# Kernel tuning notes

Measured on AMD Instinct MI355X. Metric: run time of the kernel, lower is better.

The kernel has to match this reference:

```python
import jax, jax.numpy as jnp
import numpy as np

B, LI, LT, D, H, DH, E, I, IS, TOPK = 2, 1024, 256, 768, 12, 64, 8, 3072, 1536, 2


def _rms(x, s):
    # RMSNorm over last dim, eps=1e-6, learned scale s [DH]
    r = jax.lax.rsqrt(jnp.mean(x * x, axis=-1, keepdims=True) + 1e-6)
    return x * r * s


def _ln(x):
    # LayerNorm without affine (elementwise_affine=False), eps=1e-6
    m = jnp.mean(x, axis=-1, keepdims=True)
    v = jnp.mean((x - m) ** 2, axis=-1, keepdims=True)
    return (x - m) * jax.lax.rsqrt(v + 1e-6)


def _mlp(x, wg, wu, wd):
    # SwiGLU MoeMLP: down(silu(gate(x)) * up(x))
    return (jax.nn.silu(x @ wg.T) * (x @ wu.T)) @ wd.T


def _moe(x, gw, eg, eu, ed, sg, su, sd):
    # x: [T, D]. Softmax gate -> top-k (norm_topk_prob=False -> raw weights),
    # combine expert outputs weighted by routing probs, plus shared experts.
    scores = jax.nn.softmax(x @ gw.T, axis=-1)            # [T, E]
    tw, ti = jax.lax.top_k(scores, TOPK)                  # [T, K]
    T = x.shape[0]
    w = jnp.zeros((T, E), x.dtype).at[jnp.arange(T)[:, None], ti].add(tw)
    y = jnp.zeros_like(x)
    for e in range(E):  # fixed small expert count
        y = y + w[:, e:e + 1] * _mlp(x, eg[e], eu[e], ed[e])
    return y + _mlp(x, sg, su, sd)


def _mod(vec, w, b):
    # Modulation(double=True): Linear(silu(vec)) -> 6 chunks, broadcast over seq
    return jnp.split((jax.nn.silu(vec) @ w.T + b)[:, None, :], 6, axis=-1)


def _qkv(x, w, b, qs, ks):
    Bb, L, _ = x.shape
    qkv = (x @ w.T + b).reshape(Bb, L, 3, H, DH).transpose(2, 0, 3, 1, 4)  # [3,B,H,L,DH]
    q, k, v = qkv[0], qkv[1], qkv[2]
    return _rms(q, qs), _rms(k, ks), v


def _forward(img, txt, vec, imw, imb, tmw, tmb, iqkvw, iqkvb, ipw, ipb, tqkvw, tqkvb, tpw, tpb, iqs, iks, tqs, tks, igw, ieg, ieu, ied, isg, isu, isd, tgw, teg, teu, ted, tsg, tsu, tsd):
    is1, ic1, ig1, is2, ic2, ig2 = _mod(vec, imw, imb)
    ts1, tc1, tg1, ts2, tc2, tg2 = _mod(vec, tmw, tmb)
    iq, ik, iv = _qkv((1 + ic1) * _ln(img) + is1, iqkvw, iqkvb, iqs, iks)
    tq, tk, tv = _qkv((1 + tc1) * _ln(txt) + ts1, tqkvw, tqkvb, tqs, tks)
    # joint attention over concat(txt, img)
    q = jnp.concatenate([tq, iq], axis=2)
    k = jnp.concatenate([tk, ik], axis=2)
    v = jnp.concatenate([tv, iv], axis=2)
    a = jax.nn.softmax(jnp.einsum('bhqd,bhkd->bhqk', q, k) / np.float32(np.sqrt(DH)), axis=-1)
    o = jnp.einsum('bhqk,bhkd->bhqd', a, v).transpose(0, 2, 1, 3).reshape(B, LT + LI, D)
    txt_a, img_a = o[:, :LT], o[:, LT:]
    img = img + ig1 * (img_a @ ipw.T + ipb)
    txt = txt + tg1 * (txt_a @ tpw.T + tpb)
    img = img + ig2 * _moe(((1 + ic2) * _ln(img) + is2).reshape(-1, D), igw, ieg, ieu, ied, isg, isu, isd).reshape(B, LI, D)
    txt = txt + tg2 * _moe(((1 + tc2) * _ln(txt) + ts2).reshape(-1, D), tgw, teg, teu, ted, tsg, tsu, tsd).reshape(B, LT, D)
    return img, txt


def setup_inputs() -> dict:
    key = jax.random.key(0)
    ks = jax.random.split(key, 32)
    n = lambda i, sh, s=1.0: jax.random.normal(ks[i], sh, jnp.float32) * s
    W = 0.02
    return {
        'img': n(0, (B, LI, D)), 'txt': n(1, (B, LT, D)), 'vec': n(2, (B, D)),
        'imw': n(3, (6 * D, D), W), 'imb': n(4, (6 * D,), W),
        'tmw': n(5, (6 * D, D), W), 'tmb': n(6, (6 * D,), W),
        'iqkvw': n(7, (3 * D, D), W), 'iqkvb': n(8, (3 * D,), W),
        'ipw': n(9, (D, D), W), 'ipb': n(10, (D,), W),
        'tqkvw': n(11, (3 * D, D), W), 'tqkvb': n(12, (3 * D,), W),
        'tpw': n(13, (D, D), W), 'tpb': n(14, (D,), W),
        'iqs': jnp.ones((DH,), jnp.float32), 'iks': jnp.ones((DH,), jnp.float32),
        'tqs': jnp.ones((DH,), jnp.float32), 'tks': jnp.ones((DH,), jnp.float32),
        'igw': n(15, (E, D), W), 'ieg': n(16, (E, I, D), W), 'ieu': n(17, (E, I, D), W), 'ied': n(18, (E, D, I), W),
        'isg': n(19, (IS, D), W), 'isu': n(20, (IS, D), W), 'isd': n(21, (D, IS), W),
        'tgw': n(22, (E, D), W), 'teg': n(23, (E, I, D), W), 'teu': n(24, (E, I, D), W), 'ted': n(25, (E, D, I), W),
        'tsg': n(26, (IS, D), W), 'tsu': n(27, (IS, D), W), 'tsd': n(28, (D, IS), W),
    }


def reference(img, txt, vec, imw, imb, tmw, tmb, iqkvw, iqkvb, ipw, ipb, tqkvw, tqkvb, tpw, tpb, iqs, iks, tqs, tks, igw, ieg, ieu, ied, isg, isu, isd, tgw, teg, teu, ted, tsg, tsu, tsd):
    return _forward(img, txt, vec, imw, imb, tmw, tmb, iqkvw, iqkvb, ipw, ipb, tqkvw, tqkvb, tpw, tpb, iqs, iks, tqs, tks, igw, ieg, ieu, ied, isg, isu, isd, tgw, teg, teu, ted, tsg, tsu, tsd)
```

## Files before the change

### kernel.cpp

```cpp
#include <hip/hip_runtime.h>
#include <hip/hip_bf16.h>

using bf16 = __hip_bfloat16;
typedef __attribute__((ext_vector_type(4))) float f32x4;
typedef __attribute__((ext_vector_type(8))) short s16x8;

#define DEV static __device__ __forceinline__
DEV float bf2f(bf16 x){ return __bfloat162float(x); }
DEV bf16  f2bf(float x){ return __float2bfloat16(x); }
DEV float silu_(float x){ return x / (1.f + expf(-x)); }

template<bool B_F32, bool EXPERT, bool GATHER, int OUT, bool BIAS, bool GU>
DEV void gemm_core(
    const bf16* __restrict__ A, const void* __restrict__ Bv,
    const void* __restrict__ B2v,
    const float* __restrict__ bias, void* __restrict__ C,
    int M, int N, int K, long a_zoff, long b_zoff, int bshift, int biasz,
    int zdiv, long c_so, long c_si, int ldc,
    float alpha, int ksplit, long c_spo,
    const int* __restrict__ rowlist, const int* __restrict__ offsets,
    const int* __restrict__ counts)
{
  __shared__ __align__(16) char smem_[36864];
  bf16 (*As)[72] = (bf16(*)[72])smem_;
  bf16 (*Bs)[72] = (bf16(*)[72])(smem_ + 18432);
  float (*st)[132] = (float(*)[132])smem_;

  const int zz = blockIdx.z;
  const int z = zz / ksplit, split = zz % ksplit;
  const int m0 = blockIdx.y * 128, n0 = blockIdx.x * 128;
  int Meff = M; long rowbase = 0;
  if (EXPERT){ Meff = counts[z]; rowbase = offsets[z]; }
  if (m0 >= Meff) return;
  const bf16* Ab = A + (EXPERT ? 0 : z * a_zoff);
  const int bidx = z >> bshift;
  long coff;
  if (EXPERT) coff = rowbase * (long)ldc;
  else        coff = (long)(z / zdiv) * c_so + (long)(z % zdiv) * c_si;
  coff += (long)split * c_spo;
  const float* bias_eff = BIAS ? bias + (long)bidx * biasz : nullptr;

  const int klen = K / ksplit;
  const int kbeg = split * klen;
  const int NT = klen >> 6;

  const int tid = threadIdx.x;
  const int lane = tid & 63, wid = tid >> 6;
  const int wm = wid >> 1, wn = wid & 1;

  const int rbase = tid >> 3;
  const int kc = (tid & 7) << 3;
  const bf16* ap[4];
  const bf16* bp[4];  const float* bpf[4];
  const bf16* bp2[4]; const float* bpf2[4];
  bool avalid[4], bvalid[4];
  #pragma unroll
  for (int it = 0; it < 4; it++){
    int row = rbase + 32 * it;
    long ar = 0;
    if (EXPERT){
      int i = m0 + row;
      avalid[it] = i < Meff;
      if (avalid[it]) ar = GATHER ? (long)rowlist[rowbase + i] : (rowbase + i);
    } else {
      avalid[it] = (m0 + row) < Meff;
      ar = m0 + row;
    }
    ap[it] = Ab + ar * (long)K + kbeg + kc;
    bvalid[it] = (n0 + row) < N;
    long br = bvalid[it] ? (long)(n0 + row) : 0;
    if (B_F32){
      bpf[it] = (const float*)Bv + bidx * b_zoff + br * K + kbeg + kc;
      if (GU) bpf2[it] = (const float*)B2v + bidx * b_zoff + br * K + kbeg + kc;
    } else {
      bp[it]  = (const bf16*)Bv + bidx * b_zoff + br * K + kbeg + kc;
      if (GU) bp2[it] = (const bf16*)B2v + bidx * b_zoff + br * K + kbeg + kc;
    }
  }

  uint4 ra[4], rb[4], rb2[4];
  float4 fb0[4], fb1[4], f20[4], f21[4];
  const uint4 zero4 = make_uint4(0u,0u,0u,0u);

  auto LOADA = [&](int koff){
    #pragma unroll
    for (int it = 0; it < 4; it++)
      ra[it] = avalid[it] ? *(const uint4*)(ap[it] + koff) : zero4;
  };
  auto LOADB = [&](int koff){
    #pragma unroll
    for (int it = 0; it < 4; it++){
      if (B_F32){
        if (bvalid[it]){ fb0[it] = *(const float4*)(bpf[it] + koff);
                         fb1[it] = *(const float4*)(bpf[it] + koff + 4); }
        else { fb0[it] = make_float4(0,0,0,0); fb1[it] = make_float4(0,0,0,0); }
      } else rb[it] = bvalid[it] ? *(const uint4*)(bp[it] + koff) : zero4;
    }
  };
  auto LOADB2 = [&](int koff){
    #pragma unroll
    for (int it = 0; it < 4; it++){
      if (B_F32){
        if (bvalid[it]){ f20[it] = *(const float4*)(bpf2[it] + koff);
                         f21[it] = *(const float4*)(bpf2[it] + koff + 4); }
        else { f20[it] = make_float4(0,0,0,0); f21[it] = make_float4(0,0,0,0); }
      } else rb2[it] = bvalid[it] ? *(const uint4*)(bp2[it] + koff) : zero4;
    }
  };
  auto cvt = [&](float4 a, float4 b)->uint4{
    union { bf16 h[8]; uint4 v; } u;
    u.h[0]=f2bf(a.x); u.h[1]=f2bf(a.y); u.h[2]=f2bf(a.z); u.h[3]=f2bf(a.w);
    u.h[4]=f2bf(b.x); u.h[5]=f2bf(b.y); u.h[6]=f2bf(b.z); u.h[7]=f2bf(b.w);
    return u.v;
  };
  auto STOREA = [&](){
    #pragma unroll
    for (int it = 0; it < 4; it++) *(uint4*)(&As[rbase + 32*it][kc]) = ra[it];
  };
  auto STOREB = [&](){
    #pragma unroll
    for (int it = 0; it < 4; it++)
      *(uint4*)(&Bs[rbase + 32*it][kc]) = B_F32 ? cvt(fb0[it], fb1[it]) : rb[it];
  };
  auto STOREB2 = [&](){
    #pragma unroll
    for (int it = 0; it < 4; it++)
      *(uint4*)(&Bs[rbase + 32*it][kc]) = B_F32 ? cvt(f20[it], f21[it]) : rb2[it];
  };

  f32x4 acc[4][4] = {};
  f32x4 acc2[4][4] = {};
  auto MFMA = [&](f32x4 (&ac)[4][4]){
    #pragma unroll
    for (int ks2 = 0; ks2 < 2; ks2++){
      const int r16 = lane & 15;
      const int kk = ks2 * 32 + ((lane >> 4) << 3);
      s16x8 af[4], bfr[4];
      #pragma unroll
      for (int mi = 0; mi < 4; mi++) af[mi]  = *(const s16x8*)(&As[wm*64 + mi*16 + r16][kk]);
      #pragma unroll
      for (int ni = 0; ni < 4; ni++) bfr[ni] = *(const s16x8*)(&Bs[wn*64 + ni*16 + r16][kk]);
      #pragma unroll
      for (int mi = 0; mi < 4; mi++)
        #pragma unroll
        for (int ni = 0; ni < 4; ni++)
          ac[mi][ni] = __builtin_amdgcn_mfma_f32_16x16x32_bf16(af[mi], bfr[ni], ac[mi][ni], 0, 0, 0);
    }
  };

  LOADA(0); LOADB(0);
  for (int t = 0; t < NT; t++){
    STOREA(); STOREB();
    __syncthreads();
    if (GU){
      LOADB2(t << 6);
      MFMA(acc);
      __syncthreads();
      STOREB2();
      __syncthreads();
      if (t + 1 < NT){ LOADA((t+1) << 6); LOADB((t+1) << 6); }
      MFMA(acc2);
      __syncthreads();
    } else {
      if (t + 1 < NT){ LOADA((t+1) << 6); LOADB((t+1) << 6); }
      MFMA(acc);
      __syncthreads();
    }
  }

  const int er = tid >> 3;
  const int ec = (tid & 7) << 4;
  const int erg = m0 + (er & 15) + ((er & 16) ? 64 : 0);
  #pragma unroll
  for (int mi = 0; mi < 4; mi++){
    #pragma unroll
    for (int ni = 0; ni < 4; ni++){
      int lc = wn*64 + ni*16 + (lane & 15);
      float bv = 0.f;
      if (BIAS){ if (split == 0) bv = bias_eff[n0 + lc]; }
      #pragma unroll
      for (int i = 0; i < 4; i++){
        int lr = wm*16 + ((lane >> 4) << 2) + i;
        float v;
        if (GU) v = silu_(acc[mi][ni][i]) * acc2[mi][ni][i];
        else    v = acc[mi][ni][i] * alpha + bv;
        st[lr][lc] = v;
      }
    }
    __syncthreads();
    int rg = erg + mi*16;
    int cg = n0 + ec;
    if (rg < Meff && cg < N){
      long base = coff + (long)rg * ldc + cg;
      if (OUT == 0){
        float* dst = (float*)C + base;
        #pragma unroll
        for (int q = 0; q < 4; q++)
          *(float4*)(dst + 4*q) = make_float4(st[er][ec+4*q], st[er][ec+4*q+1],
                                              st[er][ec+4*q+2], st[er][ec+4*q+3]);
      } else {
        union { bf16 h[8]; uint4 v; } o0, o1;
        #pragma unroll
        for (int j = 0; j < 8; j++){
          o0.h[j] = f2bf(st[er][ec+j]);
          o1.h[j] = f2bf(st[er][ec+8+j]);
        }
        *(uint4*)((bf16*)C + base)     = o0.v;
        *(uint4*)((bf16*)C + base + 8) = o1.v;
      }
    }
    __syncthreads();
  }
}

#define GEMM_K(NAME, BF32, EXPERT, GATHER, OUT, BIAS, GU)                          \
__global__ __launch_bounds__(256) void NAME(                                       \
    const bf16* A, const void* Bv, const void* B2v, const float* bias, void* C,    \
    int M, int N, int K, long az, long bz, int bshift, int biasz,                  \
    int zdiv, long cso, long csi, int ldc, float alpha, int ks, long cspo,         \
    const int* rl, const int* ofs, const int* cnt){                                \
  gemm_core<BF32,EXPERT,GATHER,OUT,BIAS,GU>(A,Bv,B2v,bias,C,M,N,K,az,bz,bshift,    \
      biasz,zdiv,cso,csi,ldc,alpha,ks,cspo,rl,ofs,cnt); }

GEMM_K(k_qkv_b,  false,true ,false,1,true ,false)
GEMM_K(k_qkt,    false,false,false,1,false,false)
GEMM_K(k_pv,     false,false,false,0,false,false)
GEMM_K(k_proj_b, false,true ,false,0,true ,false)
GEMM_K(k_gu_b,   false,true ,true ,1,false,true )
GEMM_K(k_down_b, false,true ,false,0,false,false)
GEMM_K(k_sgu_b,  false,true ,false,1,false,true )
GEMM_K(k_sdown_b,false,true ,false,0,false,false)
GEMM_K(k_qkv_f,  true ,true ,false,1,true ,false)
GEMM_K(k_proj_f, true ,true ,false,0,true ,false)
GEMM_K(k_gu_f,   true ,true ,true ,1,false,true )
GEMM_K(k_down_f, true ,true ,false,0,false,false)
GEMM_K(k_sgu_f,  true ,true ,false,1,false,true )
GEMM_K(k_sdown_f,true ,true ,false,0,false,false)

__global__ void init_kernel(int* cnt16, int* tabs){
  int i = threadIdx.x;
  if (i < 16) cnt16[i] = 0;
  if (i == 0){
    tabs[0]=2048; tabs[1]=512; tabs[2]=0; tabs[3]=2048;
    tabs[4]=256; tabs[5]=256; tabs[6]=1024; tabs[7]=1024;
    tabs[8]=0; tabs[9]=1280; tabs[10]=256; tabs[11]=1536;
    tabs[12]=2048; tabs[13]=512; tabs[14]=0; tabs[15]=2048;
  }
}
__global__ void tables_kernel(const int* cnt16, int* ofs16, int* cur16){
  if (threadIdx.x == 0){
    int o = 0;
    for (int e = 0; e < 8; e++){ ofs16[e] = o; o += cnt16[e]; cur16[e] = 0; }
    o = 4096;
    for (int e = 8; e < 16; e++){ ofs16[e] = o; o += cnt16[e]; cur16[e] = 0; }
  }
}

__global__ __launch_bounds__(256) void f2b_kernel(const float* __restrict__ in,
    bf16* __restrict__ out, long n){
  long i = ((long)blockIdx.x * 256 + threadIdx.x) * 8;
  if (i >= n) return;
  float4 a = *(const float4*)(in + i);
  float4 b = *(const float4*)(in + i + 4);
  union { bf16 h[8]; uint4 v; } u;
  u.h[0]=f2bf(a.x); u.h[1]=f2bf(a.y); u.h[2]=f2bf(a.z); u.h[3]=f2bf(a.w);
  u.h[4]=f2bf(b.x); u.h[5]=f2bf(b.y); u.h[6]=f2bf(b.z); u.h[7]=f2bf(b.w);
  *(uint4*)(out + i) = u.v;
}

__global__ __launch_bounds__(256) void reduce_o_kernel(const float* __restrict__ Op,
    bf16* __restrict__ O, int chunk){
  int z = blockIdx.y;
  int bh = chunk*6 + z;
  int b = bh / 12, hh = bh % 12;
  int d = threadIdx.x & 63, rr = threadIdx.x >> 6;
  const float* base = Op + (long)z * 1280 * 64;
  #pragma unroll
  for (int j = 0; j < 4; j++){
    int row = blockIdx.x * 16 + rr * 4 + j;
    float s = 0.f;
    #pragma unroll
    for (int sp = 0; sp < 10; sp++) s += base[(long)sp*6*1280*64 + (long)row*64 + d];
    O[((long)b*1280 + row)*768 + hh*64 + d] = f2bf(s);
  }
}

__global__ __launch_bounds__(256) void mod_kernel(const float* __restrict__ vec,
    const float* __restrict__ w, const float* __restrict__ b, float* __restrict__ out){
  int bb = blockIdx.y;
  __shared__ float sv[768];
  int tid = threadIdx.x;
  for (int i = tid; i < 768; i += 256){ float v = vec[bb*768 + i]; sv[i] = v/(1.f+expf(-v)); }
  __syncthreads();
  int w4 = tid >> 6, lane = tid & 63;
  int j0 = blockIdx.x * 8 + w4 * 2;
  for (int jj = 0; jj < 2; jj++){
    int j = j0 + jj;
    const float* wr = w + (long)j * 768;
    float p = 0.f;
    #pragma unroll
    for (int i = 0; i < 12; i++) p += sv[lane + 64*i] * wr[lane + 64*i];
    for (int o = 32; o; o >>= 1) p += __shfl_xor(p, o);
    if (lane == 0) out[bb*4608 + j] = p + b[j];
  }
}
// ... 156 lines not shown

__global__ __launch_bounds__(256) void scatter_kernel(const int* __restrict__ tki,
    const int* __restrict__ ofs16, int* __restrict__ cur16,
    int* __restrict__ rows16, int* __restrict__ tpos, int T, int tabofs, int rowadd){
  int idx = blockIdx.x * 256 + threadIdx.x;
  if (idx >= T * 2) return;
  int t = idx >> 1;
  int e = tki[idx];
  int pos = atomicAdd(&cur16[tabofs + e], 1);
  int g = ofs16[tabofs + e] + pos;
  rows16[g] = rowadd + t;
  tpos[idx] = g;
}

__global__ __launch_bounds__(256) void combine_kernel(const float* __restrict__ h,
    const float* __restrict__ mod, const float* __restrict__ tkw, const int* __restrict__ tpos,
    const float* __restrict__ ye, long espo, const float* __restrict__ ys, long sspo,
    float* __restrict__ out, int L){
  int t = blockIdx.x; int b = t / L;
  const float* g2 = mod + (long)b * 4608 + 5*768;
  float w0 = tkw[t*2], w1 = tkw[t*2+1];
  long p0 = (long)tpos[t*2] * 768, p1 = (long)tpos[t*2+1] * 768;
  for (int d = threadIdx.x; d < 768; d += 256){
    float e0 = ye[p0+d] + ye[espo+p0+d];
    float e1 = ye[p1+d] + ye[espo+p1+d];
    float sv = ys[(long)t*768+d] + ys[sspo+(long)t*768+d];
    out[(long)t*768 + d] = h[(long)t*768 + d] + g2[d] * (w0*e0 + w1*e1 + sv);
  }
}

extern "C" void kernel_launch(void* const* d_in, const int* in_sizes, int n_in,
                              void* d_out, int out_size, void* d_ws, size_t ws_size,
                              hipStream_t stream){
  (void)in_sizes; (void)n_in; (void)out_size;
  const float* fin[33];
  for (int i = 0; i < 33; i++) fin[i] = (const float*)d_in[i];
  float* out_img = (float*)d_out;
  float* out_txt = (float*)d_out + (long)2*1024*768;

  char* ws = (char*)d_ws;
  size_t off = 0, peak = 0;
  auto alloc = [&](size_t n)->char*{
    off = (off + 255) & ~(size_t)255;
    char* p = ws + off; off += n;
    if (off > peak) peak = off;
    return p;
  };

  float *mod_i, *mod_t, *h_i, *h_t, *x2fc, *tkw_i, *tkw_t;
  bf16 *x2c;
  int *tki_i, *tki_t, *cnt16, *ofs16, *cur16, *rows16, *tpos_i, *tpos_t, *tabs;
  float *qb_ws, *pb_ws;
  bf16 *wq=nullptr,*wp=nullptr,*wg16=nullptr,*wu16=nullptr,*wd16=nullptr,
       *wsg2=nullptr,*wsu2=nullptr,*wsd2=nullptr;
  bf16 *Qb,*Kb,*Vt,*O,*xmc,*qrc,*S,*P;
  float *pjc,*Opart;
  bf16 *h1,*h1s;
  float *ye,*ys;

  auto build = [&](bool W){
    off = 0; peak = 0;
    mod_i=(float*)alloc(2*4608*4);  mod_t=(float*)alloc(2*4608*4);
    h_i  =(float*)alloc((size_t)2048*768*4); h_t=(float*)alloc((size_t)512*768*4);
    x2c  =(bf16*) alloc((size_t)2560*768*2);
    x2fc =(float*)alloc((size_t)2560*768*4);
    tkw_i=(float*)alloc(2048*2*4); tki_i=(int*)alloc(2048*2*4);
    tkw_t=(float*)alloc(512*2*4);  tki_t=(int*)alloc(512*2*4);
    cnt16=(int*)alloc(16*4); ofs16=(int*)alloc(16*4); cur16=(int*)alloc(16*4);
    rows16=(int*)alloc(5120*4);
    tpos_i=(int*)alloc(4096*4); tpos_t=(int*)alloc(1024*4);
    tabs=(int*)alloc(64*4);
    qb_ws=(float*)alloc(2*2304*4); pb_ws=(float*)alloc(2*768*4);
    if (W){
      const size_t EB = (size_t)8*3072*768*2;
      wg16=(bf16*)alloc(2*EB); wu16=(bf16*)alloc(2*EB); wd16=(bf16*)alloc(2*EB);
      wq  =(bf16*)alloc(2*(size_t)2304*768*2);
      wp  =(bf16*)alloc(2*(size_t)768*768*2);
      wsg2=(bf16*)alloc(2*(size_t)1536*768*2);
      wsu2=(bf16*)alloc(2*(size_t)1536*768*2);
      wsd2=(bf16*)alloc(2*(size_t)768*1536*2);
    }
    size_t arena = (off + 255) & ~(size_t)255;
    off = arena;
    Qb=(bf16*)alloc((size_t)24*1280*64*2);
    Kb=(bf16*)alloc((size_t)24*1280*64*2);
    Vt=(bf16*)alloc((size_t)24*1280*64*2);
    O =(bf16*)alloc((size_t)2*1280*768*2);
    pjc=(float*)alloc((size_t)2*2560*768*4);
    size_t sub = (off + 255) & ~(size_t)255;
    xmc=(bf16*)alloc((size_t)2560*768*2);
    qrc=(bf16*)alloc((size_t)2560*2304*2);
    off = sub;
    S=(bf16*)alloc((size_t)6*1280*1280*2);
    P=(bf16*)alloc((size_t)6*1280*1280*2);
    Opart=(float*)alloc((size_t)10*6*1280*64*4);
    off = arena;
    h1 =(bf16*) alloc((size_t)5120*3072*2);
    ye =(float*)alloc((size_t)2*5120*768*4);
    h1s=(bf16*) alloc((size_t)2560*1536*2);
    ys =(float*)alloc((size_t)2*2560*768*4);
  };

  build(true);
  bool W = (peak <= ws_size);
  if (!W) build(false);

  hipMemcpyAsync(qb_ws,        fin[8],  2304*4, hipMemcpyDeviceToDevice, stream);
  hipMemcpyAsync(qb_ws+2304,   fin[12], 2304*4, hipMemcpyDeviceToDevice, stream);
  hipMemcpyAsync(pb_ws,        fin[14], 768*4,  hipMemcpyDeviceToDevice, stream);
  hipMemcpyAsync(pb_ws+768,    fin[10], 768*4,  hipMemcpyDeviceToDevice, stream);

  if (W){
    auto cv = [&](const float* src, bf16* dst, long n){
      f2b_kernel<<<(unsigned)((n/8 + 255)/256), 256, 0, stream>>>(src, dst, n);
    };
    const long EN = (long)8*3072*768;
    cv(fin[20], wg16, EN);      cv(fin[27], wg16+EN, EN);
    cv(fin[21], wu16, EN);      cv(fin[28], wu16+EN, EN);
    cv(fin[22], wd16, EN);      cv(fin[29], wd16+EN, EN);
    cv(fin[7],  wq, (long)2304*768);   cv(fin[11], wq+(long)2304*768, (long)2304*768);
    cv(fin[13], wp, (long)768*768);    cv(fin[9],  wp+(long)768*768,  (long)768*768);
    cv(fin[23], wsg2, (long)1536*768); cv(fin[30], wsg2+(long)1536*768, (long)1536*768);
    cv(fin[24], wsu2, (long)1536*768); cv(fin[31], wsu2+(long)1536*768, (long)1536*768);
    cv(fin[25], wsd2, (long)768*1536); cv(fin[32], wsd2+(long)768*1536, (long)768*1536);
  }

  init_kernel<<<1, 64, 0, stream>>>(cnt16, tabs);
  mod_kernel<<<dim3(576,2), 256, 0, stream>>>(fin[2], fin[3], fin[4], mod_i);
  mod_kernel<<<dim3(576,2), 256, 0, stream>>>(fin[2], fin[5], fin[6], mod_t);
  ln_mod_kernel<<<2048, 256, 0, stream>>>(fin[0], mod_i, xmc, 1024);
  ln_mod_kernel<<<512,  256, 0, stream>>>(fin[1], mod_t, xmc + (long)2048*768, 256);

  if (W)
    k_qkv_b<<<dim3(18,16,2), 256, 0, stream>>>(xmc, wq, nullptr, qb_ws, qrc,
        0, 2304, 768, 0, (long)2304*768, 0, 2304, 1, 0, 0, 2304, 1.f, 1, 0,
        nullptr, tabs+2, tabs+0);
  else {
    k_qkv_f<<<dim3(18,16,1), 256, 0, stream>>>(xmc, fin[7], nullptr, qb_ws, qrc,
        0, 2304, 768, 0, 0, 0, 0, 1, 0, 0, 2304, 1.f, 1, 0, nullptr, tabs+2, tabs+0);
    k_qkv_f<<<dim3(18,4,1), 256, 0, stream>>>(xmc, fin[11], nullptr, qb_ws+2304, qrc,
        0, 2304, 768, 0, 0, 0, 0, 1, 0, 0, 2304, 1.f, 1, 0, nullptr, tabs+3, tabs+1);
  }
  qkv_scatter_kernel<<<dim3(16,24), 256, 0, stream>>>(qrc, fin[15], fin[16], Qb, Kb, Vt, 1024, 256);
  qkv_scatter_kernel<<<dim3(4,24),  256, 0, stream>>>(qrc + (long)2048*2304, fin[17], fin[18], Qb, Kb, Vt, 256, 0);

  for (int ch = 0; ch < 4; ch++){
    const bf16* Qc = Qb + (size_t)ch * 6 * 1280 * 64;
    const bf16* Kc = Kb + (size_t)ch * 6 * 1280 * 64;
    const bf16* Vc = Vt + (size_t)ch * 6 * 1280 * 64;
    k_qkt<<<dim3(10,10,6), 256, 0, stream>>>(Qc, Kc, nullptr, nullptr, S,
        1280, 1280, 64, (long)1280*64, (long)1280*64, 0, 0,
        1, (long)1280*1280, 0, 1280, 0.125f, 1, 0, nullptr, nullptr, nullptr);
    softmax_kernel<<<6*1280, 256, 0, stream>>>(S, P);
    k_pv<<<dim3(1,10,60), 256, 0, stream>>>(P, Vc, nullptr, nullptr, Opart,
        1280, 64, 1280, (long)1280*1280, (long)64*1280, 0, 0,
        1, (long)1280*64, 0, 64, 1.f, 10, (long)6*1280*64, nullptr, nullptr, nullptr);
    reduce_o_kernel<<<dim3(80,6), 256, 0, stream>>>(Opart, O, ch);
  }

  if (W)
    k_proj_b<<<dim3(6,8,8), 256, 0, stream>>>(O, wp, nullptr, pb_ws, pjc,
        0, 768, 768, 0, (long)768*768, 1, 768, 1, 0, 0, 768, 1.f, 2, (long)2560*768,
        nullptr, tabs+8, tabs+4);
  else {
    k_proj_f<<<dim3(6,2,4), 256, 0, stream>>>(O, fin[13], nullptr, pb_ws, pjc,
        0, 768, 768, 0, 0, 1, 0, 1, 0, 0, 768, 1.f, 2, (long)2560*768,
        nullptr, tabs+8, tabs+4);
    k_proj_f<<<dim3(6,8,4), 256, 0, stream>>>(O, fin[9], nullptr, pb_ws+768, pjc,
        0, 768, 768, 0, 0, 1, 0, 1, 0, 0, 768, 1.f, 2, (long)2560*768,
        nullptr, tabs+10, tabs+6);
  }
  resid_ln_mod_kernel<<<2048, 256, 0, stream>>>(fin[0], pjc, 256, (long)2560*768,
      mod_i, h_i, x2c, x2fc, 1024);
  resid_ln_mod_kernel<<<512, 256, 0, stream>>>(fin[1], pjc, 0, (long)2560*768,
      mod_t, h_t, x2c + (long)2048*768, x2fc + (long)2048*768, 256);

  router_kernel<<<512, 256, 0, stream>>>(x2fc, fin[19], tkw_i, tki_i, cnt16, 2048);
  router_kernel<<<128, 256, 0, stream>>>(x2fc + (long)2048*768, fin[26], tkw_t, tki_t, cnt16+8, 512);
  tables_kernel<<<1, 1, 0, stream>>>(cnt16, ofs16, cur16);
  scatter_kernel<<<16, 256, 0, stream>>>(tki_i, ofs16, cur16, rows16, tpos_i, 2048, 0, 0);
  scatter_kernel<<<4,  256, 0, stream>>>(tki_t, ofs16, cur16, rows16, tpos_t, 512, 8, 2048);

  if (W){
    k_gu_b<<<dim3(24,16,16), 256, 0, stream>>>(x2c, wg16, wu16, nullptr, h1,
        0, 3072, 768, 0, (long)3072*768, 0, 0, 1, 0, 0, 3072, 1.f, 1, 0,
        rows16, ofs16, cnt16);
    k_down_b<<<dim3(6,16,32), 256, 0, stream>>>(h1, wd16, nullptr, nullptr, ye,
        0, 768, 3072, 0, (long)768*3072, 0, 0, 1, 0, 0, 768, 1.f, 2, (long)5120*768,
        nullptr, ofs16, cnt16);
    k_sgu_b<<<dim3(12,16,2), 256, 0, stream>>>(x2c, wsg2, wsu2, nullptr, h1s,
        0, 1536, 768, 0, (long)1536*768, 0, 0, 1, 0, 0, 1536, 1.f, 1, 0,
        nullptr, tabs+14, tabs+12);
    k_sdown_b<<<dim3(6,16,4), 256, 0, stream>>>(h1s, wsd2, nullptr, nullptr, ys,
        0, 768, 1536, 0, (long)768*1536, 0, 0, 1, 0, 0, 768, 1.f, 2, (long)2560*768,
        nullptr, tabs+14, tabs+12);
  } else {
    k_gu_f<<<dim3(24,16,8), 256, 0, stream>>>(x2c, fin[20], fin[21], nullptr, h1,
        0, 3072, 768, 0, (long)3072*768, 0, 0, 1, 0, 0, 3072, 1.f, 1, 0,
        rows16, ofs16, cnt16);
    k_gu_f<<<dim3(24,16,8), 256, 0, stream>>>(x2c, fin[27], fin[28], nullptr, h1,
        0, 3072, 768, 0, (long)3072*768, 0, 0, 1, 0, 0, 3072, 1.f, 1, 0,
        rows16, ofs16+8, cnt16+8);
    k_down_f<<<dim3(6,16,16), 256, 0, stream>>>(h1, fin[22], nullptr, nullptr, ye,
        0, 768, 3072, 0, (long)768*3072, 0, 0, 1, 0, 0, 768, 1.f, 2, (long)5120*768,
        nullptr, ofs16, cnt16);
    k_down_f<<<dim3(6,16,16), 256, 0, stream>>>(h1, fin[29], nullptr, nullptr, ye,
        0, 768, 3072, 0, (long)768*3072, 0, 0, 1, 0, 0, 768, 1.f, 2, (long)5120*768,
        nullptr, ofs16+8, cnt16+8);
    k_sgu_f<<<dim3(12,16,1), 256, 0, stream>>>(x2c, fin[23], fin[24], nullptr, h1s,
        0, 1536, 768, 0, 0, 0, 0, 1, 0, 0, 1536, 1.f, 1, 0, nullptr, tabs+14, tabs+12);
    k_sgu_f<<<dim3(12,4,1), 256, 0, stream>>>(x2c, fin[30], fin[31], nullptr, h1s,
        0, 1536, 768, 0, 0, 0, 0, 1, 0, 0, 1536, 1.f, 1, 0, nullptr, tabs+15, tabs+13);
    k_sdown_f<<<dim3(6,16,2), 256, 0, stream>>>(h1s, fin[25], nullptr, nullptr, ys,
        0, 768, 1536, 0, 0, 0, 0, 1, 0, 0, 768, 1.f, 2, (long)2560*768,
        nullptr, tabs+14, tabs+12);
    k_sdown_f<<<dim3(6,4,2), 256, 0, stream>>>(h1s, fin[32], nullptr, nullptr, ys,
        0, 768, 1536, 0, 0, 0, 0, 1, 0, 0, 768, 1.f, 2, (long)2560*768,
        nullptr, tabs+15, tabs+13);
  }
  combine_kernel<<<2048, 256, 0, stream>>>(h_i, mod_i, tkw_i, tpos_i,
      ye, (long)5120*768, ys, (long)2560*768, out_img, 1024);
  combine_kernel<<<512, 256, 0, stream>>>(h_t, mod_t, tkw_t, tpos_t,
      ye, (long)5120*768, ys + (long)2048*768, (long)2560*768, out_txt, 256);
}
```

Before: 1.161 ms.

## Drop bf16 weight pre-conversion; concat gate/up GEMM and fuse SwiGLU into down loads

Removes the workspace-dependent path that converted all fp32 weights to bf16 in separate kernels; every GEMM now reads fp32 weights and converts while staging to shared memory. Gate and up projections become one wider GEMM whose B rows select between the two weight tensors, and the SwiGLU activation moves into the A-tile load of the down projection, which now uses 4-way split-K. Attention runs in 2 chunks of 12 heads with softmax in place and 5-way PV split-K. This drops a large conversion pass and the dual-accumulator loop, but every GEMM tile rereads fp32 weights and the down GEMM recomputes silu per load.

```diff
diff --git a/kernel.cpp b/kernel.cpp
--- a/kernel.cpp
+++ b/kernel.cpp
@@ -10,12 +10,14 @@
 DEV bf16  f2bf(float x){ return __float2bfloat16(x); }
 DEV float silu_(float x){ return x / (1.f + expf(-x)); }
 
-template<bool B_F32, bool EXPERT, bool GATHER, int OUT, bool BIAS, bool GU>
+template<bool B_F32, bool EXPERT, bool GATHER, int OUT, bool BIAS, bool FUSE>
 DEV void gemm_core(
-    const bf16* __restrict__ A, const void* __restrict__ Bv,
-    const void* __restrict__ B2v,
+    const bf16* __restrict__ A,
+    const void* __restrict__ B0a, const void* __restrict__ B0b,
+    const void* __restrict__ B1a, const void* __restrict__ B1b,
     const float* __restrict__ bias, void* __restrict__ C,
-    int M, int N, int K, long a_zoff, long b_zoff, int bshift, int biasz,
+    int M, int N, int K, int lda, int fuseOff,
+    long a_zoff, long b_zoff, int bshift, int biasz, int nsplitB,
     int zdiv, long c_so, long c_si, int ldc,
     float alpha, int ksplit, long c_spo,
     const int* __restrict__ rowlist, const int* __restrict__ offsets,
@@ -34,6 +36,9 @@
   if (m0 >= Meff) return;
   const bf16* Ab = A + (EXPERT ? 0 : z * a_zoff);
   const int bidx = z >> bshift;
+  const long e = (long)(z & ((1 << bshift) - 1));
+  const void* BL = bidx ? B1a : B0a;
+  const void* BU = bidx ? B1b : B0b;
   long coff;
   if (EXPERT) coff = rowbase * (long)ldc;
   else        coff = (long)(z / zdiv) * c_so + (long)(z % zdiv) * c_si;
@@ -50,9 +55,8 @@
 
   const int rbase = tid >> 3;
   const int kc = (tid & 7) << 3;
-  const bf16* ap[4];
-  const bf16* bp[4];  const float* bpf[4];
-  const bf16* bp2[4]; const float* bpf2[4];
+  const bf16* ap[4]; const bf16* ap2[4];
+  const bf16* bp[4]; const float* bpf[4];
   bool avalid[4], bvalid[4];
   #pragma unroll
   for (int it = 0; it < 4; it++){
@@ -66,71 +70,67 @@
       avalid[it] = (m0 + row) < Meff;
       ar = m0 + row;
     }
-    ap[it] = Ab + ar * (long)K + kbeg + kc;
-    bvalid[it] = (n0 + row) < N;
-    long br = bvalid[it] ? (long)(n0 + row) : 0;
-    if (B_F32){
-      bpf[it] = (const float*)Bv + bidx * b_zoff + br * K + kbeg + kc;
-      if (GU) bpf2[it] = (const float*)B2v + bidx * b_zoff + br * K + kbeg + kc;
-    } else {
-      bp[it]  = (const bf16*)Bv + bidx * b_zoff + br * K + kbeg + kc;
-      if (GU) bp2[it] = (const bf16*)B2v + bidx * b_zoff + br * K + kbeg + kc;
-    }
-  }
-
-  uint4 ra[4], rb[4], rb2[4];
-  float4 fb0[4], fb1[4], f20[4], f21[4];
+    ap[it] = Ab + ar * (long)lda + kbeg + kc;
+    if (FUSE) ap2[it] = ap[it] + fuseOff;
+    int br = n0 + row;
+    bvalid[it] = br < N;
+    int brc = bvalid[it] ? br : 0;
+    bool up = brc >= nsplitB;
+    long brr = up ? (brc - nsplitB) : brc;
+    const void* Bsel = up ? BU : BL;
+    if (B_F32) bpf[it] = (const float*)Bsel + e * b_zoff + brr * K + kbeg + kc;
+    else       bp[it]  = (const bf16*) Bsel + e * b_zoff + brr * K + kbeg + kc;
+  }
+
+  uint4 ra[4], ru[4], rb[4];
+  float4 fb0[4], fb1[4];
   const uint4 zero4 = make_uint4(0u,0u,0u,0u);
 
-  auto LOADA = [&](int koff){
-    #pragma unroll
-    for (int it = 0; it < 4; it++)
+  auto LOAD = [&](int koff){
+    #pragma unroll
+    for (int it = 0; it < 4; it++){
       ra[it] = avalid[it] ? *(const uint4*)(ap[it] + koff) : zero4;
-  };
-  auto LOADB = [&](int koff){
-    #pragma unroll
-    for (int it = 0; it < 4; it++){
+      if (FUSE) ru[it] = avalid[it] ? *(const uint4*)(ap2[it] + koff) : zero4;
       if (B_F32){
         if (bvalid[it]){ fb0[it] = *(const float4*)(bpf[it] + koff);
                          fb1[it] = *(const float4*)(bpf[it] + koff + 4); }
         else { fb0[it] = make_float4(0,0,0,0); fb1[it] = make_float4(0,0,0,0); }
-      } else rb[it] = bvalid[it] ? *(const uint4*)(bp[it] + koff) : zero4;
+      } else {
+        rb[it] = bvalid[it] ? *(const uint4*)(bp[it] + koff) : zero4;
+      }
     }
   };
-  auto LOADB2 = [&](int koff){
+  auto STORE = [&](){
     #pragma unroll
     for (int it = 0; it < 4; it++){
+      int row = rbase + 32 * it;
+      uint4 av = ra[it];
+      if (FUSE){
+        union { bf16 h[8]; uint4 v; } g_, u_, r_;
+        g_.v = ra[it]; u_.v = ru[it];
+        #pragma unroll
+        for (int j = 0; j < 8; j++)
+          r_.h[j] = f2bf(silu_(bf2f(g_.h[j])) * bf2f(u_.h[j]));
+        av = r_.v;
+      }
+      *(uint4*)(&As[row][kc]) = av;
       if (B_F32){
-        if (bvalid[it]){ f20[it] = *(const float4*)(bpf2[it] + koff);
-                         f21[it] = *(const float4*)(bpf2[it] + koff + 4); }
-        else { f20[it] = make_float4(0,0,0,0); f21[it] = make_float4(0,0,0,0); }
-      } else rb2[it] = bvalid[it] ? *(const uint4*)(bp2[it] + koff) : zero4;
+        union { bf16 h[8]; uint4 v; } u;
+        u.h[0]=f2bf(fb0[it].x); u.h[1]=f2bf(fb0[it].y); u.h[2]=f2bf(fb0[it].z); u.h[3]=f2bf(fb0[it].w);
+        u.h[4]=f2bf(fb1[it].x); u.h[5]=f2bf(fb1[it].y); u.h[6]=f2bf(fb1[it].z); u.h[7]=f2bf(fb1[it].w);
+        *(uint4*)(&Bs[row][kc]) = u.v;
+      } else {
+        *(uint4*)(&Bs[row][kc]) = rb[it];
+      }
     }
   };
-  auto cvt = [&](float4 a, float4 b)->uint4{
-    union { bf16 h[8]; uint4 v; } u;
-    u.h[0]=f2bf(a.x); u.h[1]=f2bf(a.y); u.h[2]=f2bf(a.z); u.h[3]=f2bf(a.w);
-    u.h[4]=f2bf(b.x); u.h[5]=f2bf(b.y); u.h[6]=f2bf(b.z); u.h[7]=f2bf(b.w);
-    return u.v;
-  };
-  auto STOREA = [&](){
-    #pragma unroll
-    for (int it = 0; it < 4; it++) *(uint4*)(&As[rbase + 32*it][kc]) = ra[it];
-  };
-  auto STOREB = [&](){
-    #pragma unroll
-    for (int it = 0; it < 4; it++)
-      *(uint4*)(&Bs[rbase + 32*it][kc]) = B_F32 ? cvt(fb0[it], fb1[it]) : rb[it];
-  };
-  auto STOREB2 = [&](){
-    #pragma unroll
-    for (int it = 0; it < 4; it++)
-      *(uint4*)(&Bs[rbase + 32*it][kc]) = B_F32 ? cvt(f20[it], f21[it]) : rb2[it];
-  };
 
   f32x4 acc[4][4] = {};
-  f32x4 acc2[4][4] = {};
-  auto MFMA = [&](f32x4 (&ac)[4][4]){
+  LOAD(0);
+  for (int t = 0; t < NT; t++){
+    STORE();
+    __syncthreads();
+    if (t + 1 < NT) LOAD((t + 1) << 6);
     #pragma unroll
     for (int ks2 = 0; ks2 < 2; ks2++){
       const int r16 = lane & 15;
@@ -144,28 +144,9 @@
       for (int mi = 0; mi < 4; mi++)
         #pragma unroll
         for (int ni = 0; ni < 4; ni++)
-          ac[mi][ni] = __builtin_amdgcn_mfma_f32_16x16x32_bf16(af[mi], bfr[ni], ac[mi][ni], 0, 0, 0);
-    }
-  };
-
-  LOADA(0); LOADB(0);
-  for (int t = 0; t < NT; t++){
-    STOREA(); STOREB();
+          acc[mi][ni] = __builtin_amdgcn_mfma_f32_16x16x32_bf16(af[mi], bfr[ni], acc[mi][ni], 0, 0, 0);
+    }
     __syncthreads();
-    if (GU){
-      LOADB2(t << 6);
-      MFMA(acc);
-      __syncthreads();
-      STOREB2();
-      __syncthreads();
-      if (t + 1 < NT){ LOADA((t+1) << 6); LOADB((t+1) << 6); }
-      MFMA(acc2);
-      __syncthreads();
-    } else {
-      if (t + 1 < NT){ LOADA((t+1) << 6); LOADB((t+1) << 6); }
-      MFMA(acc);
-      __syncthreads();
-    }
   }
 
   const int er = tid >> 3;
@@ -181,10 +162,7 @@
       #pragma unroll
       for (int i = 0; i < 4; i++){
         int lr = wm*16 + ((lane >> 4) << 2) + i;
-        float v;
-        if (GU) v = silu_(acc[mi][ni][i]) * acc2[mi][ni][i];
-        else    v = acc[mi][ni][i] * alpha + bv;
-        st[lr][lc] = v;
+        st[lr][lc] = acc[mi][ni][i] * alpha + bv;
       }
     }
     __syncthreads();
@@ -213,29 +191,24 @@
   }
 }
 
-#define GEMM_K(NAME, BF32, EXPERT, GATHER, OUT, BIAS, GU)                          \
+#define GEMM_K(NAME, BF32, EXPERT, GATHER, OUT, BIAS, FUSE)                        \
 __global__ __launch_bounds__(256) void NAME(                                       \
-    const bf16* A, const void* Bv, const void* B2v, const float* bias, void* C,    \
-    int M, int N, int K, long az, long bz, int bshift, int biasz,                  \
-    int zdiv, long cso, long csi, int ldc, float alpha, int ks, long cspo,         \
-    const int* rl, const int* ofs, const int* cnt){                                \
-  gemm_core<BF32,EXPERT,GATHER,OUT,BIAS,GU>(A,Bv,B2v,bias,C,M,N,K,az,bz,bshift,    \
-      biasz,zdiv,cso,csi,ldc,alpha,ks,cspo,rl,ofs,cnt); }
-
-GEMM_K(k_qkv_b,  false,true ,false,1,true ,false)
-GEMM_K(k_qkt,    false,false,false,1,false,false)
-GEMM_K(k_pv,     false,false,false,0,false,false)
-GEMM_K(k_proj_b, false,true ,false,0,true ,false)
-GEMM_K(k_gu_b,   false,true ,true ,1,false,true )
-GEMM_K(k_down_b, false,true ,false,0,false,false)
-GEMM_K(k_sgu_b,  false,true ,false,1,false,true )
-GEMM_K(k_sdown_b,false,true ,false,0,false,false)
-GEMM_K(k_qkv_f,  true ,true ,false,1,true ,false)
-GEMM_K(k_proj_f, true ,true ,false,0,true ,false)
-GEMM_K(k_gu_f,   true ,true ,true ,1,false,true )
-GEMM_K(k_down_f, true ,true ,false,0,false,false)
-GEMM_K(k_sgu_f,  true ,true ,false,1,false,true )
-GEMM_K(k_sdown_f,true ,true ,false,0,false,false)
+    const bf16* A, const void* B0a, const void* B0b, const void* B1a,              \
+    const void* B1b, const float* bias, void* C,                                   \
+    int M, int N, int K, int lda, int fo, long az, long bz, int bshift, int biasz, \
+    int nsplitB, int zdiv, long cso, long csi, int ldc, float alpha, int ks,       \
+    long cspo, const int* rl, const int* ofs, const int* cnt){                     \
+  gemm_core<BF32,EXPERT,GATHER,OUT,BIAS,FUSE>(A,B0a,B0b,B1a,B1b,bias,C,M,N,K,lda,  \
+      fo,az,bz,bshift,biasz,nsplitB,zdiv,cso,csi,ldc,alpha,ks,cspo,rl,ofs,cnt); }
+
+GEMM_K(k_qkv,  true ,true ,false,1,true ,false)
+GEMM_K(k_qkt,  false,false,false,1,false,false)
+GEMM_K(k_pv,   false,false,false,0,false,false)
+GEMM_K(k_proj, true ,true ,false,0,true ,false)
+GEMM_K(k_gup,  true ,true ,true ,1,false,false)
+GEMM_K(k_down, true ,true ,false,0,false,true )
+GEMM_K(k_sgup, true ,true ,false,1,false,false)
+GEMM_K(k_sdown,true ,true ,false,0,false,true )
 
 __global__ void init_kernel(int* cnt16, int* tabs){
   int i = threadIdx.x;
@@ -256,31 +229,19 @@
   }
 }
 
-__global__ __launch_bounds__(256) void f2b_kernel(const float* __restrict__ in,
-    bf16* __restrict__ out, long n){
-  long i = ((long)blockIdx.x * 256 + threadIdx.x) * 8;
-  if (i >= n) return;
-  float4 a = *(const float4*)(in + i);
-  float4 b = *(const float4*)(in + i + 4);
-  union { bf16 h[8]; uint4 v; } u;
-  u.h[0]=f2bf(a.x); u.h[1]=f2bf(a.y); u.h[2]=f2bf(a.z); u.h[3]=f2bf(a.w);
-  u.h[4]=f2bf(b.x); u.h[5]=f2bf(b.y); u.h[6]=f2bf(b.z); u.h[7]=f2bf(b.w);
-  *(uint4*)(out + i) = u.v;
-}
-
 __global__ __launch_bounds__(256) void reduce_o_kernel(const float* __restrict__ Op,
     bf16* __restrict__ O, int chunk){
-  int z = blockIdx.y;
-  int bh = chunk*6 + z;
+  int zh = blockIdx.y;
+  int bh = chunk*12 + zh;
   int b = bh / 12, hh = bh % 12;
   int d = threadIdx.x & 63, rr = threadIdx.x >> 6;
-  const float* base = Op + (long)z * 1280 * 64;
+  const float* base = Op + (long)zh * 1280 * 64;
   #pragma unroll
   for (int j = 0; j < 4; j++){
     int row = blockIdx.x * 16 + rr * 4 + j;
     float s = 0.f;
     #pragma unroll
-    for (int sp = 0; sp < 10; sp++) s += base[(long)sp*6*1280*64 + (long)row*64 + d];
+    for (int sp = 0; sp < 5; sp++) s += base[(long)sp*12*1280*64 + (long)row*64 + d];
     O[((long)b*1280 + row)*768 + hh*64 + d] = f2bf(s);
   }
 }
@@ -483,9 +444,14 @@
   float w0 = tkw[t*2], w1 = tkw[t*2+1];
   long p0 = (long)tpos[t*2] * 768, p1 = (long)tpos[t*2+1] * 768;
   for (int d = threadIdx.x; d < 768; d += 256){
-    float e0 = ye[p0+d] + ye[espo+p0+d];
-    float e1 = ye[p1+d] + ye[espo+p1+d];
-    float sv = ys[(long)t*768+d] + ys[sspo+(long)t*768+d];
+    float e0 = 0.f, e1 = 0.f, sv = 0.f;
+    #pragma unroll
+    for (int sp = 0; sp < 4; sp++){
+      e0 += ye[sp*espo + p0 + d];
+      e1 += ye[sp*espo + p1 + d];
+    }
+    #pragma unroll
+    for (int sp = 0; sp < 2; sp++) sv += ys[sp*sspo + (long)t*768 + d];
     out[(long)t*768 + d] = h[(long)t*768 + d] + g2[d] * (w0*e0 + w1*e1 + sv);
   }
 }
@@ -493,98 +459,62 @@
 extern "C" void kernel_launch(void* const* d_in, const int* in_sizes, int n_in,
                               void* d_out, int out_size, void* d_ws, size_t ws_size,
                               hipStream_t stream){
-  (void)in_sizes; (void)n_in; (void)out_size;
+  (void)in_sizes; (void)n_in; (void)out_size; (void)ws_size;
   const float* fin[33];
   for (int i = 0; i < 33; i++) fin[i] = (const float*)d_in[i];
   float* out_img = (float*)d_out;
   float* out_txt = (float*)d_out + (long)2*1024*768;
 
   char* ws = (char*)d_ws;
-  size_t off = 0, peak = 0;
+  size_t off = 0;
   auto alloc = [&](size_t n)->char*{
     off = (off + 255) & ~(size_t)255;
-    char* p = ws + off; off += n;
-    if (off > peak) peak = off;
-    return p;
+    char* p = ws + off; off += n; return p;
   };
 
-  float *mod_i, *mod_t, *h_i, *h_t, *x2fc, *tkw_i, *tkw_t;
-  bf16 *x2c;
-  int *tki_i, *tki_t, *cnt16, *ofs16, *cur16, *rows16, *tpos_i, *tpos_t, *tabs;
-  float *qb_ws, *pb_ws;
-  bf16 *wq=nullptr,*wp=nullptr,*wg16=nullptr,*wu16=nullptr,*wd16=nullptr,
-       *wsg2=nullptr,*wsu2=nullptr,*wsd2=nullptr;
-  bf16 *Qb,*Kb,*Vt,*O,*xmc,*qrc,*S,*P;
-  float *pjc,*Opart;
-  bf16 *h1,*h1s;
-  float *ye,*ys;
-
-  auto build = [&](bool W){
-    off = 0; peak = 0;
-    mod_i=(float*)alloc(2*4608*4);  mod_t=(float*)alloc(2*4608*4);
-    h_i  =(float*)alloc((size_t)2048*768*4); h_t=(float*)alloc((size_t)512*768*4);
-    x2c  =(bf16*) alloc((size_t)2560*768*2);
-    x2fc =(float*)alloc((size_t)2560*768*4);
-    tkw_i=(float*)alloc(2048*2*4); tki_i=(int*)alloc(2048*2*4);
-    tkw_t=(float*)alloc(512*2*4);  tki_t=(int*)alloc(512*2*4);
-    cnt16=(int*)alloc(16*4); ofs16=(int*)alloc(16*4); cur16=(int*)alloc(16*4);
-    rows16=(int*)alloc(5120*4);
-    tpos_i=(int*)alloc(4096*4); tpos_t=(int*)alloc(1024*4);
-    tabs=(int*)alloc(64*4);
-    qb_ws=(float*)alloc(2*2304*4); pb_ws=(float*)alloc(2*768*4);
-    if (W){
-      const size_t EB = (size_t)8*3072*768*2;
-      wg16=(bf16*)alloc(2*EB); wu16=(bf16*)alloc(2*EB); wd16=(bf16*)alloc(2*EB);
-      wq  =(bf16*)alloc(2*(size_t)2304*768*2);
-      wp  =(bf16*)alloc(2*(size_t)768*768*2);
-      wsg2=(bf16*)alloc(2*(size_t)1536*768*2);
-      wsu2=(bf16*)alloc(2*(size_t)1536*768*2);
-      wsd2=(bf16*)alloc(2*(size_t)768*1536*2);
-    }
-    size_t arena = (off + 255) & ~(size_t)255;
-    off = arena;
-    Qb=(bf16*)alloc((size_t)24*1280*64*2);
-    Kb=(bf16*)alloc((size_t)24*1280*64*2);
-    Vt=(bf16*)alloc((size_t)24*1280*64*2);
-    O =(bf16*)alloc((size_t)2*1280*768*2);
-    pjc=(float*)alloc((size_t)2*2560*768*4);
-    size_t sub = (off + 255) & ~(size_t)255;
-    xmc=(bf16*)alloc((size_t)2560*768*2);
-    qrc=(bf16*)alloc((size_t)2560*2304*2);
-    off = sub;
-    S=(bf16*)alloc((size_t)6*1280*1280*2);
-    P=(bf16*)alloc((size_t)6*1280*1280*2);
-    Opart=(float*)alloc((size_t)10*6*1280*64*4);
-    off = arena;
-    h1 =(bf16*) alloc((size_t)5120*3072*2);
-    ye =(float*)alloc((size_t)2*5120*768*4);
-    h1s=(bf16*) alloc((size_t)2560*1536*2);
-    ys =(float*)alloc((size_t)2*2560*768*4);
-  };
-
-  build(true);
-  bool W = (peak <= ws_size);
-  if (!W) build(false);
-
-  hipMemcpyAsync(qb_ws,        fin[8],  2304*4, hipMemcpyDeviceToDevice, stream);
-  hipMemcpyAsync(qb_ws+2304,   fin[12], 2304*4, hipMemcpyDeviceToDevice, stream);
-  hipMemcpyAsync(pb_ws,        fin[14], 768*4,  hipMemcpyDeviceToDevice, stream);
-  hipMemcpyAsync(pb_ws+768,    fin[10], 768*4,  hipMemcpyDeviceToDevice, stream);
-
-  if (W){
-    auto cv = [&](const float* src, bf16* dst, long n){
-      f2b_kernel<<<(unsigned)((n/8 + 255)/256), 256, 0, stream>>>(src, dst, n);
-    };
-    const long EN = (long)8*3072*768;
-    cv(fin[20], wg16, EN);      cv(fin[27], wg16+EN, EN);
-    cv(fin[21], wu16, EN);      cv(fin[28], wu16+EN, EN);
-    cv(fin[22], wd16, EN);      cv(fin[29], wd16+EN, EN);
-    cv(fin[7],  wq, (long)2304*768);   cv(fin[11], wq+(long)2304*768, (long)2304*768);
-    cv(fin[13], wp, (long)768*768);    cv(fin[9],  wp+(long)768*768,  (long)768*768);
-    cv(fin[23], wsg2, (long)1536*768); cv(fin[30], wsg2+(long)1536*768, (long)1536*768);
-    cv(fin[24], wsu2, (long)1536*768); cv(fin[31], wsu2+(long)1536*768, (long)1536*768);
-    cv(fin[25], wsd2, (long)768*1536); cv(fin[32], wsd2+(long)768*1536, (long)768*1536);
-  }
+  float* mod_i=(float*)alloc(2*4608*4);
+  float* mod_t=(float*)alloc(2*4608*4);
+  float* h_i  =(float*)alloc((size_t)2048*768*4);
+  float* h_t  =(float*)alloc((size_t)512*768*4);
+  bf16*  x2c  =(bf16*) alloc((size_t)2560*768*2);
+  float* x2fc =(float*)alloc((size_t)2560*768*4);
+  float* tkw_i=(float*)alloc(2048*2*4);
+  int*   tki_i=(int*)  alloc(2048*2*4);
+  float* tkw_t=(float*)alloc(512*2*4);
+  int*   tki_t=(int*)  alloc(512*2*4);
+  int* cnt16=(int*)alloc(16*4);
+  int* ofs16=(int*)alloc(16*4);
+  int* cur16=(int*)alloc(16*4);
+  int* rows16=(int*)alloc(5120*4);
+  int* tpos_i=(int*)alloc(4096*4);
+  int* tpos_t=(int*)alloc(1024*4);
+  int* tabs=(int*)alloc(64*4);
+  float* qb_ws=(float*)alloc(2*2304*4);
+  float* pb_ws=(float*)alloc(2*768*4);
+
+  size_t arena = (off + 255) & ~(size_t)255;
+  off = arena;
+  bf16* Qb=(bf16*)alloc((size_t)24*1280*64*2);
+  bf16* Kb=(bf16*)alloc((size_t)24*1280*64*2);
+  bf16* Vt=(bf16*)alloc((size_t)24*1280*64*2);
+  bf16* O =(bf16*)alloc((size_t)2*1280*768*2);
+  float* pjc=(float*)alloc((size_t)2*2560*768*4);
+  size_t sub = (off + 255) & ~(size_t)255;
+  bf16* xmc=(bf16*)alloc((size_t)2560*768*2);
+  bf16* qrc=(bf16*)alloc((size_t)2560*2304*2);
+  off = sub;
+  bf16* S=(bf16*)alloc((size_t)12*1280*1280*2);
+  float* Opart=(float*)alloc((size_t)5*12*1280*64*4);
+  off = arena;
+  bf16*  h1gu =(bf16*) alloc((size_t)5120*6144*2);
+  float* ye   =(float*)alloc((size_t)4*5120*768*4);
+  bf16*  h1sgu=(bf16*) alloc((size_t)2560*3072*2);
+  float* ys   =(float*)alloc((size_t)2*2560*768*4);
+
+  hipMemcpyAsync(qb_ws,      fin[8],  2304*4, hipMemcpyDeviceToDevice, stream);
+  hipMemcpyAsync(qb_ws+2304, fin[12], 2304*4, hipMemcpyDeviceToDevice, stream);
+  hipMemcpyAsync(pb_ws,      fin[14], 768*4,  hipMemcpyDeviceToDevice, stream);
+  hipMemcpyAsync(pb_ws+768,  fin[10], 768*4,  hipMemcpyDeviceToDevice, stream);
 
   init_kernel<<<1, 64, 0, stream>>>(cnt16, tabs);
   mod_kernel<<<dim3(576,2), 256, 0, stream>>>(fin[2], fin[3], fin[4], mod_i);
@@ -592,45 +522,29 @@
   ln_mod_kernel<<<2048, 256, 0, stream>>>(fin[0], mod_i, xmc, 1024);
   ln_mod_kernel<<<512,  256, 0, stream>>>(fin[1], mod_t, xmc + (long)2048*768, 256);
 
-  if (W)
-    k_qkv_b<<<dim3(18,16,2), 256, 0, stream>>>(xmc, wq, nullptr, qb_ws, qrc,
-        0, 2304, 768, 0, (long)2304*768, 0, 2304, 1, 0, 0, 2304, 1.f, 1, 0,
-        nullptr, tabs+2, tabs+0);
-  else {
-    k_qkv_f<<<dim3(18,16,1), 256, 0, stream>>>(xmc, fin[7], nullptr, qb_ws, qrc,
-        0, 2304, 768, 0, 0, 0, 0, 1, 0, 0, 2304, 1.f, 1, 0, nullptr, tabs+2, tabs+0);
-    k_qkv_f<<<dim3(18,4,1), 256, 0, stream>>>(xmc, fin[11], nullptr, qb_ws+2304, qrc,
-        0, 2304, 768, 0, 0, 0, 0, 1, 0, 0, 2304, 1.f, 1, 0, nullptr, tabs+3, tabs+1);
-  }
+  k_qkv<<<dim3(18,16,2), 256, 0, stream>>>(xmc, fin[7], fin[7], fin[11], fin[11],
+      qb_ws, qrc, 0, 2304, 768, 768, 0, 0, 0, 0, 2304, 2304,
+      1, 0, 0, 2304, 1.f, 1, 0, nullptr, tabs+2, tabs+0);
   qkv_scatter_kernel<<<dim3(16,24), 256, 0, stream>>>(qrc, fin[15], fin[16], Qb, Kb, Vt, 1024, 256);
   qkv_scatter_kernel<<<dim3(4,24),  256, 0, stream>>>(qrc + (long)2048*2304, fin[17], fin[18], Qb, Kb, Vt, 256, 0);
 
-  for (int ch = 0; ch < 4; ch++){
-    const bf16* Qc = Qb + (size_t)ch * 6 * 1280 * 64;
-    const bf16* Kc = Kb + (size_t)ch * 6 * 1280 * 64;
-    const bf16* Vc = Vt + (size_t)ch * 6 * 1280 * 64;
-    k_qkt<<<dim3(10,10,6), 256, 0, stream>>>(Qc, Kc, nullptr, nullptr, S,
-        1280, 1280, 64, (long)1280*64, (long)1280*64, 0, 0,
+  for (int ch = 0; ch < 2; ch++){
+    const bf16* Qc = Qb + (size_t)ch * 12 * 1280 * 64;
+    const bf16* Kc = Kb + (size_t)ch * 12 * 1280 * 64;
+    const bf16* Vc = Vt + (size_t)ch * 12 * 1280 * 64;
+    k_qkt<<<dim3(10,10,12), 256, 0, stream>>>(Qc, Kc, Kc, Kc, Kc, nullptr, S,
+        1280, 1280, 64, 64, 0, (long)1280*64, (long)1280*64, 30, 0, 1280,
         1, (long)1280*1280, 0, 1280, 0.125f, 1, 0, nullptr, nullptr, nullptr);
-    softmax_kernel<<<6*1280, 256, 0, stream>>>(S, P);
-    k_pv<<<dim3(1,10,60), 256, 0, stream>>>(P, Vc, nullptr, nullptr, Opart,
-        1280, 64, 1280, (long)1280*1280, (long)64*1280, 0, 0,
-        1, (long)1280*64, 0, 64, 1.f, 10, (long)6*1280*64, nullptr, nullptr, nullptr);
-    reduce_o_kernel<<<dim3(80,6), 256, 0, stream>>>(Opart, O, ch);
-  }
-
-  if (W)
-    k_proj_b<<<dim3(6,8,8), 256, 0, stream>>>(O, wp, nullptr, pb_ws, pjc,
-        0, 768, 768, 0, (long)768*768, 1, 768, 1, 0, 0, 768, 1.f, 2, (long)2560*768,
-        nullptr, tabs+8, tabs+4);
-  else {
-    k_proj_f<<<dim3(6,2,4), 256, 0, stream>>>(O, fin[13], nullptr, pb_ws, pjc,
-        0, 768, 768, 0, 0, 1, 0, 1, 0, 0, 768, 1.f, 2, (long)2560*768,
-        nullptr, tabs+8, tabs+4);
-    k_proj_f<<<dim3(6,8,4), 256, 0, stream>>>(O, fin[9], nullptr, pb_ws+768, pjc,
-        0, 768, 768, 0, 0, 1, 0, 1, 0, 0, 768, 1.f, 2, (long)2560*768,
-        nullptr, tabs+10, tabs+6);
-  }
+    softmax_kernel<<<12*1280, 256, 0, stream>>>(S, S);
+    k_pv<<<dim3(1,10,60), 256, 0, stream>>>(S, Vc, Vc, Vc, Vc, nullptr, Opart,
+        1280, 64, 1280, 1280, 0, (long)1280*1280, (long)64*1280, 30, 0, 64,
+        1, (long)1280*64, 0, 64, 1.f, 5, (long)12*1280*64, nullptr, nullptr, nullptr);
+    reduce_o_kernel<<<dim3(80,12), 256, 0, stream>>>(Opart, O, ch);
+  }
+
+  k_proj<<<dim3(6,8,8), 256, 0, stream>>>(O, fin[13], fin[13], fin[9], fin[9],
+      pb_ws, pjc, 0, 768, 768, 768, 0, 0, 0, 1, 768, 768,
+      1, 0, 0, 768, 1.f, 2, (long)2560*768, nullptr, tabs+8, tabs+4);
   resid_ln_mod_kernel<<<2048, 256, 0, stream>>>(fin[0], pjc, 256, (long)2560*768,
       mod_i, h_i, x2c, x2fc, 1024);
   resid_ln_mod_kernel<<<512, 256, 0, stream>>>(fin[1], pjc, 0, (long)2560*768,
@@ -642,43 +556,19 @@
   scatter_kernel<<<16, 256, 0, stream>>>(tki_i, ofs16, cur16, rows16, tpos_i, 2048, 0, 0);
   scatter_kernel<<<4,  256, 0, stream>>>(tki_t, ofs16, cur16, rows16, tpos_t, 512, 8, 2048);
 
-  if (W){
-    k_gu_b<<<dim3(24,16,16), 256, 0, stream>>>(x2c, wg16, wu16, nullptr, h1,
-        0, 3072, 768, 0, (long)3072*768, 0, 0, 1, 0, 0, 3072, 1.f, 1, 0,
-        rows16, ofs16, cnt16);
-    k_down_b<<<dim3(6,16,32), 256, 0, stream>>>(h1, wd16, nullptr, nullptr, ye,
-        0, 768, 3072, 0, (long)768*3072, 0, 0, 1, 0, 0, 768, 1.f, 2, (long)5120*768,
-        nullptr, ofs16, cnt16);
-    k_sgu_b<<<dim3(12,16,2), 256, 0, stream>>>(x2c, wsg2, wsu2, nullptr, h1s,
-        0, 1536, 768, 0, (long)1536*768, 0, 0, 1, 0, 0, 1536, 1.f, 1, 0,
-        nullptr, tabs+14, tabs+12);
-    k_sdown_b<<<dim3(6,16,4), 256, 0, stream>>>(h1s, wsd2, nullptr, nullptr, ys,
-        0, 768, 1536, 0, (long)768*1536, 0, 0, 1, 0, 0, 768, 1.f, 2, (long)2560*768,
-        nullptr, tabs+14, tabs+12);
-  } else {
-    k_gu_f<<<dim3(24,16,8), 256, 0, stream>>>(x2c, fin[20], fin[21], nullptr, h1,
-        0, 3072, 768, 0, (long)3072*768, 0, 0, 1, 0, 0, 3072, 1.f, 1, 0,
-        rows16, ofs16, cnt16);
-    k_gu_f<<<dim3(24,16,8), 256, 0, stream>>>(x2c, fin[27], fin[28], nullptr, h1,
-        0, 3072, 768, 0, (long)3072*768, 0, 0, 1, 0, 0, 3072, 1.f, 1, 0,
-        rows16, ofs16+8, cnt16+8);
-    k_down_f<<<dim3(6,16,16), 256, 0, stream>>>(h1, fin[22], nullptr, nullptr, ye,
-        0, 768, 3072, 0, (long)768*3072, 0, 0, 1, 0, 0, 768, 1.f, 2, (long)5120*768,
-        nullptr, ofs16, cnt16);
-    k_down_f<<<dim3(6,16,16), 256, 0, stream>>>(h1, fin[29], nullptr, nullptr, ye,
-        0, 768, 3072, 0, (long)768*3072, 0, 0, 1, 0, 0, 768, 1.f, 2, (long)5120*768,
-        nullptr, ofs16+8, cnt16+8);
-    k_sgu_f<<<dim3(12,16,1), 256, 0, stream>>>(x2c, fin[23], fin[24], nullptr, h1s,
-        0, 1536, 768, 0, 0, 0, 0, 1, 0, 0, 1536, 1.f, 1, 0, nullptr, tabs+14, tabs+12);
-    k_sgu_f<<<dim3(12,4,1), 256, 0, stream>>>(x2c, fin[30], fin[31], nullptr, h1s,
-        0, 1536, 768, 0, 0, 0, 0, 1, 0, 0, 1536, 1.f, 1, 0, nullptr, tabs+15, tabs+13);
-    k_sdown_f<<<dim3(6,16,2), 256, 0, stream>>>(h1s, fin[25], nullptr, nullptr, ys,
-        0, 768, 1536, 0, 0, 0, 0, 1, 0, 0, 768, 1.f, 2, (long)2560*768,
-        nullptr, tabs+14, tabs+12);
-    k_sdown_f<<<dim3(6,4,2), 256, 0, stream>>>(h1s, fin[32], nullptr, nullptr, ys,
-        0, 768, 1536, 0, 0, 0, 0, 1, 0, 0, 768, 1.f, 2, (long)2560*768,
-        nullptr, tabs+15, tabs+13);
-  }
+  k_gup<<<dim3(48,16,16), 256, 0, stream>>>(x2c, fin[20], fin[21], fin[27], fin[28],
+      nullptr, h1gu, 0, 6144, 768, 768, 0, 0, (long)3072*768, 3, 0, 3072,
+      1, 0, 0, 6144, 1.f, 1, 0, rows16, ofs16, cnt16);
+  k_down<<<dim3(6,16,64), 256, 0, stream>>>(h1gu, fin[22], fin[22], fin[29], fin[29],
+      nullptr, ye, 0, 768, 3072, 6144, 3072, 0, (long)768*3072, 3, 0, 768,
+      1, 0, 0, 768, 1.f, 4, (long)5120*768, nullptr, ofs16, cnt16);
+  k_sgup<<<dim3(24,16,2), 256, 0, stream>>>(x2c, fin[23], fin[24], fin[30], fin[31],
+      nullptr, h1sgu, 0, 3072, 768, 768, 0, 0, 0, 0, 0, 1536,
+      1, 0, 0, 3072, 1.f, 1, 0, nullptr, tabs+14, tabs+12);
+  k_sdown<<<dim3(6,16,4), 256, 0, stream>>>(h1sgu, fin[25], fin[25], fin[32], fin[32],
+      nullptr, ys, 0, 768, 1536, 3072, 1536, 0, 0, 0, 0, 768,
+      1, 0, 0, 768, 1.f, 2, (long)2560*768, nullptr, tabs+14, tabs+12);
+
   combine_kernel<<<2048, 256, 0, stream>>>(h_i, mod_i, tkw_i, tpos_i,
       ye, (long)5120*768, ys, (long)2560*768, out_img, 1024);
   combine_kernel<<<512, 256, 0, stream>>>(h_t, mod_t, tkw_t, tpos_t,
```

Result: no change. 1.162 ms (+0.1%).
